# Kernel optimization log

Hardware: AMD Instinct MI355X
Metric: run time of the kernel (lower is better)

Reference implementation:

```python
import jax, jax.numpy as jnp
import numpy as np

N_EMBD = 1024
N_HEAD = 64

def setup_inputs() -> dict:
    key = jax.random.key(0)
    ks = jax.random.split(key, 7)
    B, T = 4, 4096
    x = jax.random.normal(ks[0], (B, T, N_EMBD), dtype=jnp.float32)
    # causal mask: True above the diagonal (masked positions)
    mask = jnp.triu(jnp.ones((T, T), dtype=bool), k=1)
    s = 1.0 / np.sqrt(N_EMBD)
    Wq = jax.random.normal(ks[1], (N_EMBD, N_HEAD), dtype=jnp.float32) * s
    bq = jnp.zeros((N_HEAD,), dtype=jnp.float32)
    Wk = jax.random.normal(ks[2], (N_EMBD, N_HEAD), dtype=jnp.float32) * s
    bk = jnp.zeros((N_HEAD,), dtype=jnp.float32)
    Wv = jax.random.normal(ks[3], (N_EMBD, N_HEAD), dtype=jnp.float32) * s
    bv = jnp.zeros((N_HEAD,), dtype=jnp.float32)
    return {"x": x, "mask": mask, "Wq": Wq, "bq": bq, "Wk": Wk, "bk": bk, "Wv": Wv, "bv": bv}

def reference(x, mask, Wq, bq, Wk, bk, Wv, bv):
    # x: [B,T,C], mask: [T,T] bool (True = masked)
    q = x @ Wq + bq            # [B,T,H]
    k = x @ Wk + bk            # [B,T,H]
    v = x @ Wv + bv            # [B,T,H]
    scale = 1.0 / jnp.sqrt(jnp.asarray(q.shape[-1], dtype=q.dtype))
    att = jnp.einsum('bth,bsh->bts', q, k) * scale   # [B,T,T]
    att = jnp.where(mask[None, :, :], -jnp.inf, att)
    att = jax.nn.softmax(att, axis=-1)
    # dropout omitted (eval mode / deterministic reference)
    return jnp.einsum('bts,bsh->bth', att, v)        # [B,T,H]
```

## Files before the change

### kernel.cpp

```cpp
#include <hip/hip_runtime.h>
#include <hip/hip_bf16.h>

#define BB 4
#define TT 4096
#define CC 1024
#define HH 64

#define QSCALE 0.18033688011112042f
#define FIXMAX2 23.083120654223414f

typedef __attribute__((ext_vector_type(8))) short short8;
typedef __attribute__((ext_vector_type(8))) ushort ushortx8;
typedef __attribute__((ext_vector_type(4))) float floatx4;

__device__ __forceinline__ ushort f2bf(float f) {
    union { float f; unsigned u; } a; a.f = f;
    const unsigned u = a.u;
    return (ushort)((u + 0x7fffu + ((u >> 16) & 1u)) >> 16);
}
__device__ __forceinline__ float bf2f(ushort h) {
    union { unsigned u; float f; } a; a.u = ((unsigned)h) << 16; return a.f;
}
__device__ __forceinline__ void load_lds16(const ushort* g, ushort* l) {
    __builtin_amdgcn_global_load_lds(
        (const __attribute__((address_space(1))) unsigned int*)g,
        (__attribute__((address_space(3))) unsigned int*)l, 16, 0, 0);
}

__global__ __launch_bounds__(256)
void wtrans_kernel(const float* __restrict__ Wq, const float* __restrict__ Wk,
                   const float* __restrict__ Wv, ushort* __restrict__ wT)
{
    __shared__ ushort tile[64 * 72];
    const int tid = threadIdx.x;
    const int mat = blockIdx.x >> 4, kt = blockIdx.x & 15;
    const float* W = (mat == 0) ? Wq : (mat == 1) ? Wk : Wv;
    #pragma unroll
    for (int it = 0; it < 16; ++it) {
        const int idx = it * 256 + tid;
        const int r = idx >> 6, c = idx & 63;
        tile[c * 72 + r] = f2bf(W[(size_t)(kt * 64 + r) * 64 + c]);
    }
    __syncthreads();
    #pragma unroll
    for (int it = 0; it < 16; ++it) {
        const int idx = it * 256 + tid;
        const int n = idx >> 6, kk = idx & 63;
        wT[((size_t)mat * 64 + n) * 1024 + kt * 64 + kk] = tile[n * 72 + kk];
    }
}

__global__ __launch_bounds__(256)
void qkv_mfma_kernel(const float* __restrict__ x, const ushort* __restrict__ wT,
                     const float* __restrict__ bq, const float* __restrict__ bk,
                     const float* __restrict__ bv,
                     ushort* __restrict__ q, ushort* __restrict__ k,
                     ushort* __restrict__ vT)
{
    __shared__ ushort xs [2][32 * 72];
    __shared__ ushort ws_[2][192 * 64];

    const int tid = threadIdx.x, w = tid >> 6, lane = tid & 63;
    const int m = lane & 15, quad = lane >> 4;
    const int row0 = blockIdx.x * 32;

    floatx4 acc[2][3];
    #pragma unroll
    for (int mi = 0; mi < 2; ++mi)
        #pragma unroll
        for (int j = 0; j < 3; ++j) acc[mi][j] = (floatx4){0.f, 0.f, 0.f, 0.f};

    const int lrow = lane >> 3;
    const int lg   = (lane & 7) ^ lrow;
    const ushort* gw = wT + (size_t)(w * 48 + lrow) * 1024 + lg * 8;

    const int xr = tid >> 3, xseg = tid & 7;
    const float* gx = x + (size_t)(row0 + xr) * CC + xseg * 8;

    int bslot[3][2];
    #pragma unroll
    for (int j = 0; j < 3; ++j)
        #pragma unroll
        for (int ks_ = 0; ks_ < 2; ++ks_)
            bslot[j][ks_] = ((w * 48 + j * 16 + m) * 8 +
                             ((ks_ * 4 + quad) ^ (m & 7))) * 8;

    {
        const float4 xa = *(const float4*)(gx);
        const float4 xb = *(const float4*)(gx + 4);
        #pragma unroll
        for (int j = 0; j < 6; ++j)
            load_lds16(gw + (size_t)j * 8192, &ws_[0][w * 3072 + j * 512]);
        ushortx8 p;
        p[0] = f2bf(xa.x); p[1] = f2bf(xa.y); p[2] = f2bf(xa.z); p[3] = f2bf(xa.w);
        p[4] = f2bf(xb.x); p[5] = f2bf(xb.y); p[6] = f2bf(xb.z); p[7] = f2bf(xb.w);
        *(ushortx8*)(&xs[0][xr * 72 + xseg * 8]) = p;
    }
    __syncthreads();

    for (int kc = 0; kc < 16; ++kc) {
        const int cur = kc & 1;
        float4 na, nb;
        if (kc < 15) {
            const int k0n = (kc + 1) * 64;
            na = *(const float4*)(gx + k0n);
            nb = *(const float4*)(gx + k0n + 4);
            #pragma unroll
            for (int j = 0; j < 6; ++j)
                load_lds16(gw + (size_t)j * 8192 + k0n, &ws_[cur ^ 1][w * 3072 + j * 512]);
        }
        const ushort* xb_ = xs[cur];
        const ushort* wb_ = ws_[cur];
        short8 bfr[3][2];
        #pragma unroll
        for (int j = 0; j < 3; ++j)
            #pragma unroll
            for (int ks_ = 0; ks_ < 2; ++ks_)
                bfr[j][ks_] = *(const short8*)(wb_ + bslot[j][ks_]);
        #pragma unroll
        for (int mi = 0; mi < 2; ++mi) {
            const short8 a0 = *(const short8*)(xb_ + (mi * 16 + m) * 72 + quad * 8);
            const short8 a1 = *(const short8*)(xb_ + (mi * 16 + m) * 72 + 32 + quad * 8);
            #pragma unroll
            for (int j = 0; j < 3; ++j) {
                acc[mi][j] = __builtin_amdgcn_mfma_f32_16x16x32_bf16(a0, bfr[j][0], acc[mi][j], 0, 0, 0);
                acc[mi][j] = __builtin_amdgcn_mfma_f32_16x16x32_bf16(a1, bfr[j][1], acc[mi][j], 0, 0, 0);
            }
        }
        if (kc < 15) {
            ushortx8 p;
            p[0] = f2bf(na.x); p[1] = f2bf(na.y); p[2] = f2bf(na.z); p[3] = f2bf(na.w);
            p[4] = f2bf(nb.x); p[5] = f2bf(nb.y); p[6] = f2bf(nb.z); p[7] = f2bf(nb.w);
            *(ushortx8*)(&xs[cur ^ 1][xr * 72 + xseg * 8]) = p;
        }
        __syncthreads();
    }

    const int b_ = row0 >> 12, tb = row0 & (TT - 1);
    #pragma unroll
    for (int j = 0; j < 3; ++j) {
        const int nt = w * 3 + j;
        const int mat = nt >> 2;
        const int c = (nt & 3) * 16 + m;
        const float bias = (mat == 0) ? bq[c] : (mat == 1) ? bk[c] : bv[c];
        #pragma unroll
        for (int mi = 0; mi < 2; ++mi) {
            const int gr0 = row0 + mi * 16 + quad * 4;
            if (mat == 0) {
                #pragma unroll
                for (int r = 0; r < 4; ++r)
                    q[(size_t)(gr0 + r) * HH + c] = f2bf((acc[mi][j][r] + bias) * QSCALE);
            } else if (mat == 1) {
                #pragma unroll
                for (int r = 0; r < 4; ++r)
                    k[(size_t)(gr0 + r) * HH + c] = f2bf(acc[mi][j][r] + bias);
            } else {
                ushort4 pv;
                pv.x = f2bf(acc[mi][j][0] + bias); pv.y = f2bf(acc[mi][j][1] + bias);
                pv.z = f2bf(acc[mi][j][2] + bias); pv.w = f2bf(acc[mi][j][3] + bias);
                const int t0 = tb + mi * 16 + quad * 4;
                *(ushort4*)(vT + ((size_t)b_ * HH + c) * TT + t0) = pv;
            }
        }
    }
}

__global__ __launch_bounds__(256)
void attn_mfma_kernel(const ushort* __restrict__ q, const ushort* __restrict__ k,
                      const ushort* __restrict__ vT,
                      float* __restrict__ partL, ushort* __restrict__ partO)
{
    __shared__ ushort ks[64 * 72];
    __shared__ ushort vs[64 * 72];
    __shared__ ushort ps[4][16 * 72];

    const int tid = threadIdx.x, w = tid >> 6, lane = tid & 63;
    const int m = lane & 15, quad = lane >> 4;
    const int pid = blockIdx.x;
    const int job = pid >> 3, split = pid & 7;
    const int b = job >> 6, tile = job & 63;
    const int i0 = tile * 64;
    const int nch = tile + 1;
    const int lo = (nch * split) >> 3, hi = (nch * (split + 1)) >> 3;

    const size_t qrow = ((size_t)b * TT + i0 + w * 16 + m) * HH;
    const uint4 aq0u = *(const uint4*)(q + qrow + quad * 8);
    const uint4 aq1u = *(const uint4*)(q + qrow + 32 + quad * 8);
    const short8 aq0 = *(const short8*)&aq0u;
    const short8 aq1 = *(const short8*)&aq1u;

    float lrow[4] = {0.f, 0.f, 0.f, 0.f};
    floatx4 oacc[4];
    #pragma unroll
    for (int nt = 0; nt < 4; ++nt) oacc[nt] = (floatx4){0.f, 0.f, 0.f, 0.f};

    const int iq0 = i0 + w * 16;
    for (int ch = lo; ch < hi; ++ch) {
        const int s0 = ch * 64;
        __syncthreads();
        const size_t kb = ((size_t)b * TT + s0) * HH;
        #pragma unroll
        for (int it = 0; it < 2; ++it) {
            const int t2 = it * 256 + tid;
            const int r = t2 >> 3, seg = t2 & 7;
            *(uint4*)(ks + r * 72 + seg * 8) = *(const uint4*)(k + kb + (size_t)r * HH + seg * 8);
            *(uint4*)(vs + r * 72 + seg * 8) = *(const uint4*)(vT + ((size_t)b * HH + r) * TT + s0 + seg * 8);
        }
        __syncthreads();

        floatx4 sc[4];
        #pragma unroll
        for (int nt = 0; nt < 4; ++nt) {
            const short8 b0 = *(const short8*)(ks + (nt * 16 + m) * 72 + quad * 8);
            const short8 b1 = *(const short8*)(ks + (nt * 16 + m) * 72 + 32 + quad * 8);
            floatx4 s_ = (floatx4){0.f, 0.f, 0.f, 0.f};
            s_ = __builtin_amdgcn_mfma_f32_16x16x32_bf16(aq0, b0, s_, 0, 0, 0);
            s_ = __builtin_amdgcn_mfma_f32_16x16x32_bf16(aq1, b1, s_, 0, 0, 0);
            sc[nt] = s_;
        }

        const bool need_mask = (s0 + 63 > iq0);
        #pragma unroll
        for (int r = 0; r < 4; ++r) {
            float t0 = sc[0][r] - FIXMAX2;
            float t1 = sc[1][r] - FIXMAX2;
            float t2 = sc[2][r] - FIXMAX2;
            float t3 = sc[3][r] - FIXMAX2;
            if (need_mask) {
                const int dlim = iq0 + quad * 4 + r - s0 - m;
                if (0  > dlim) t0 = -1e30f;
                if (16 > dlim) t1 = -1e30f;
                if (32 > dlim) t2 = -1e30f;
                if (48 > dlim) t3 = -1e30f;
            }
            const float p0 = __builtin_amdgcn_exp2f(t0);
            const float p1 = __builtin_amdgcn_exp2f(t1);
            const float p2 = __builtin_amdgcn_exp2f(t2);
            const float p3 = __builtin_amdgcn_exp2f(t3);
            lrow[r] += (p0 + p1) + (p2 + p3);
            ushort* pr = ps[w] + (quad * 4 + r) * 72;
            pr[m]      = f2bf(p0);
            pr[16 + m] = f2bf(p1);
            pr[32 + m] = f2bf(p2);
            pr[48 + m] = f2bf(p3);
        }

        #pragma unroll
        for (int ks_ = 0; ks_ < 2; ++ks_) {
            const short8 ap = *(const short8*)(ps[w] + m * 72 + ks_ * 32 + quad * 8);
            #pragma unroll
            for (int nt = 0; nt < 4; ++nt) {
                const short8 bv_ = *(const short8*)(vs + (nt * 16 + m) * 72 + ks_ * 32 + quad * 8);
                oacc[nt] = __builtin_amdgcn_mfma_f32_16x16x32_bf16(ap, bv_, oacc[nt], 0, 0, 0);
            }
        }
    }

    #pragma unroll
    for (int r = 0; r < 4; ++r) {
        float s = lrow[r];
        s += __shfl_xor(s, 1); s += __shfl_xor(s, 2);
        s += __shfl_xor(s, 4); s += __shfl_xor(s, 8);
        lrow[r] = s;
    }
    if (m == 0) {
        #pragma unroll
        for (int r = 0; r < 4; ++r)
            partL[(size_t)pid * 64 + w * 16 + quad * 4 + r] = lrow[r];
    }
    ushort* po = partO + ((size_t)pid * 64 + w * 16) * 64;
    #pragma unroll
    for (int r = 0; r < 4; ++r) {
        const int row = quad * 4 + r;
        #pragma unroll
        for (int nt = 0; nt < 4; ++nt)
            po[row * 64 + nt * 16 + m] = f2bf(oacc[nt][r]);
    }
}

__global__ __launch_bounds__(256)
void attn_combine_kernel(const float* __restrict__ partL,
                         const ushort* __restrict__ partO, float* __restrict__ out)
{
    const int job = blockIdx.x;
    const int tid = threadIdx.x;
    const int row = tid >> 2, dq = tid & 3;

    float L = 0.f;
    #pragma unroll
    for (int s = 0; s < 8; ++s) L += partL[(size_t)(job * 8 + s) * 64 + row];
    const float inv = 1.f / L;

    float o[16];
    #pragma unroll
    for (int i = 0; i < 16; ++i) o[i] = 0.f;
    #pragma unroll
    for (int s = 0; s < 8; ++s) {
        const ushort* po = partO + (((size_t)(job * 8 + s) * 64 + row) * 64 + dq * 16);
        #pragma unroll
        for (int i2 = 0; i2 < 2; ++i2) {
            const ushort4 pa = *(const ushort4*)(po + i2 * 8);
            const ushort4 pb = *(const ushort4*)(po + i2 * 8 + 4);
            o[i2*8+0] += bf2f(pa.x); o[i2*8+1] += bf2f(pa.y);
            o[i2*8+2] += bf2f(pa.z); o[i2*8+3] += bf2f(pa.w);
            o[i2*8+4] += bf2f(pb.x); o[i2*8+5] += bf2f(pb.y);
            o[i2*8+6] += bf2f(pb.z); o[i2*8+7] += bf2f(pb.w);
        }
    }
    float4* dst = (float4*)(out + ((size_t)job * 64 + row) * 64 + dq * 16);
    #pragma unroll
    for (int i = 0; i < 4; ++i) {
        float4 v; v.x = o[i*4]*inv; v.y = o[i*4+1]*inv; v.z = o[i*4+2]*inv; v.w = o[i*4+3]*inv;
        dst[i] = v;
    }
}

extern "C" void kernel_launch(void* const* d_in, const int* in_sizes, int n_in,
                              void* d_out, int out_size, void* d_ws, size_t ws_size,
                              hipStream_t stream) {
    (void)in_sizes; (void)n_in; (void)out_size; (void)ws_size;
    const float* x  = (const float*)d_in[0];
    const float* Wq = (const float*)d_in[2];
    const float* bq = (const float*)d_in[3];
    const float* Wk = (const float*)d_in[4];
    const float* bk = (const float*)d_in[5];
    const float* Wv = (const float*)d_in[6];
    const float* bv = (const float*)d_in[7];
    float* out = (float*)d_out;

    char* ws = (char*)d_ws;
    ushort* wT    = (ushort*)ws;
    ushort* qb    = (ushort*)(ws + 393216);
    ushort* kb    = qb + (size_t)BB * TT * HH;
    ushort* vTb   = kb + (size_t)BB * TT * HH;
    float*  partL = (float*) (ws + 6684672);
    ushort* partO = (ushort*)(ws + 7208960);

    wtrans_kernel   <<<48, 256, 0, stream>>>(Wq, Wk, Wv, wT);
    qkv_mfma_kernel <<<(BB * TT) / 32, 256, 0, stream>>>(x, wT, bq, bk, bv, qb, kb, vTb);
    attn_mfma_kernel<<<BB * 64 * 8, 256, 0, stream>>>(qb, kb, vTb, partL, partO);
    attn_combine_kernel<<<BB * 64, 256, 0, stream>>>(partL, partO, out);
}
```

Before: 200.3 us.

## Pre-swizzle weights into MFMA fragment order and load B fragments directly to registers

The weight transpose kernel now writes bf16 weights already arranged in per-lane MFMA B-fragment order. The QKV projection kernel reads these fragments straight from global memory into registers, double-buffered across k-chunks, instead of staging them through LDS with global_load_lds and swizzled reads. This removes the LDS traffic and LDS footprint for weights but adds register pressure and relies on L2 hits for the weight reads repeated by every block. The transpose kernel does uncoalesced strided reads, but it is small.

```diff
diff --git a/kernel.cpp b/kernel.cpp
--- a/kernel.cpp
+++ b/kernel.cpp
@@ -21,44 +21,41 @@
 __device__ __forceinline__ float bf2f(ushort h) {
     union { unsigned u; float f; } a; a.u = ((unsigned)h) << 16; return a.f;
 }
-__device__ __forceinline__ void load_lds16(const ushort* g, ushort* l) {
-    __builtin_amdgcn_global_load_lds(
-        (const __attribute__((address_space(1))) unsigned int*)g,
-        (__attribute__((address_space(3))) unsigned int*)l, 16, 0, 0);
-}
 
 __global__ __launch_bounds__(256)
 void wtrans_kernel(const float* __restrict__ Wq, const float* __restrict__ Wk,
-                   const float* __restrict__ Wv, ushort* __restrict__ wT)
+                   const float* __restrict__ Wv, ushort* __restrict__ wTf)
 {
-    __shared__ ushort tile[64 * 72];
     const int tid = threadIdx.x;
-    const int mat = blockIdx.x >> 4, kt = blockIdx.x & 15;
-    const float* W = (mat == 0) ? Wq : (mat == 1) ? Wk : Wv;
-    #pragma unroll
-    for (int it = 0; it < 16; ++it) {
-        const int idx = it * 256 + tid;
-        const int r = idx >> 6, c = idx & 63;
-        tile[c * 72 + r] = f2bf(W[(size_t)(kt * 64 + r) * 64 + c]);
-    }
-    __syncthreads();
-    #pragma unroll
-    for (int it = 0; it < 16; ++it) {
-        const int idx = it * 256 + tid;
-        const int n = idx >> 6, kk = idx & 63;
-        wT[((size_t)mat * 64 + n) * 1024 + kt * 64 + kk] = tile[n * 72 + kk];
+    const int kc = blockIdx.x;
+    #pragma unroll
+    for (int it = 0; it < 6; ++it) {
+        const int s = it * 256 + tid;
+        const int lane = s & 63;
+        const int t = s >> 6;
+        const int j = t % 3;
+        const int qv = t / 3;
+        const int wv = qv & 3, ks = qv >> 2;
+        const int r = wv * 48 + j * 16 + (lane & 15);
+        const int mat = r >> 6, n = r & 63;
+        const int k0 = kc * 64 + ks * 32 + (lane >> 4) * 8;
+        const float* W = (mat == 0) ? Wq : (mat == 1) ? Wk : Wv;
+        ushortx8 o;
+        #pragma unroll
+        for (int e = 0; e < 8; ++e)
+            o[e] = f2bf(W[(size_t)(k0 + e) * 64 + n]);
+        *(ushortx8*)(wTf + ((size_t)(kc * 24 + t) * 64 + lane) * 8) = o;
     }
 }
 
 __global__ __launch_bounds__(256)
-void qkv_mfma_kernel(const float* __restrict__ x, const ushort* __restrict__ wT,
+void qkv_mfma_kernel(const float* __restrict__ x, const ushort* __restrict__ wTf,
                      const float* __restrict__ bq, const float* __restrict__ bk,
                      const float* __restrict__ bv,
                      ushort* __restrict__ q, ushort* __restrict__ k,
                      ushort* __restrict__ vT)
 {
-    __shared__ ushort xs [2][32 * 72];
-    __shared__ ushort ws_[2][192 * 64];
+    __shared__ ushort xs[2][32 * 72];
 
     const int tid = threadIdx.x, w = tid >> 6, lane = tid & 63;
     const int m = lane & 15, quad = lane >> 4;
@@ -70,27 +67,21 @@
         #pragma unroll
         for (int j = 0; j < 3; ++j) acc[mi][j] = (floatx4){0.f, 0.f, 0.f, 0.f};
 
-    const int lrow = lane >> 3;
-    const int lg   = (lane & 7) ^ lrow;
-    const ushort* gw = wT + (size_t)(w * 48 + lrow) * 1024 + lg * 8;
+    const ushort* gb = wTf + (size_t)w * 1536 + lane * 8;
 
     const int xr = tid >> 3, xseg = tid & 7;
     const float* gx = x + (size_t)(row0 + xr) * CC + xseg * 8;
 
-    int bslot[3][2];
+    short8 bcur[3][2], bnxt[3][2];
+
     #pragma unroll
     for (int j = 0; j < 3; ++j)
         #pragma unroll
         for (int ks_ = 0; ks_ < 2; ++ks_)
-            bslot[j][ks_] = ((w * 48 + j * 16 + m) * 8 +
-                             ((ks_ * 4 + quad) ^ (m & 7))) * 8;
-
+            bcur[j][ks_] = *(const short8*)(gb + ks_ * 6144 + j * 512);
     {
         const float4 xa = *(const float4*)(gx);
         const float4 xb = *(const float4*)(gx + 4);
-        #pragma unroll
-        for (int j = 0; j < 6; ++j)
-            load_lds16(gw + (size_t)j * 8192, &ws_[0][w * 3072 + j * 512]);
         ushortx8 p;
         p[0] = f2bf(xa.x); p[1] = f2bf(xa.y); p[2] = f2bf(xa.z); p[3] = f2bf(xa.w);
         p[4] = f2bf(xb.x); p[5] = f2bf(xb.y); p[6] = f2bf(xb.z); p[7] = f2bf(xb.w);
@@ -105,26 +96,22 @@
             const int k0n = (kc + 1) * 64;
             na = *(const float4*)(gx + k0n);
             nb = *(const float4*)(gx + k0n + 4);
+            const ushort* gn = gb + (size_t)(kc + 1) * 12288;
             #pragma unroll
-            for (int j = 0; j < 6; ++j)
-                load_lds16(gw + (size_t)j * 8192 + k0n, &ws_[cur ^ 1][w * 3072 + j * 512]);
+            for (int j = 0; j < 3; ++j)
+                #pragma unroll
+                for (int ks_ = 0; ks_ < 2; ++ks_)
+                    bnxt[j][ks_] = *(const short8*)(gn + ks_ * 6144 + j * 512);
         }
         const ushort* xb_ = xs[cur];
-        const ushort* wb_ = ws_[cur];
-        short8 bfr[3][2];
-        #pragma unroll
-        for (int j = 0; j < 3; ++j)
-            #pragma unroll
-            for (int ks_ = 0; ks_ < 2; ++ks_)
-                bfr[j][ks_] = *(const short8*)(wb_ + bslot[j][ks_]);
         #pragma unroll
         for (int mi = 0; mi < 2; ++mi) {
             const short8 a0 = *(const short8*)(xb_ + (mi * 16 + m) * 72 + quad * 8);
             const short8 a1 = *(const short8*)(xb_ + (mi * 16 + m) * 72 + 32 + quad * 8);
             #pragma unroll
             for (int j = 0; j < 3; ++j) {
-                acc[mi][j] = __builtin_amdgcn_mfma_f32_16x16x32_bf16(a0, bfr[j][0], acc[mi][j], 0, 0, 0);
-                acc[mi][j] = __builtin_amdgcn_mfma_f32_16x16x32_bf16(a1, bfr[j][1], acc[mi][j], 0, 0, 0);
+                acc[mi][j] = __builtin_amdgcn_mfma_f32_16x16x32_bf16(a0, bcur[j][0], acc[mi][j], 0, 0, 0);
+                acc[mi][j] = __builtin_amdgcn_mfma_f32_16x16x32_bf16(a1, bcur[j][1], acc[mi][j], 0, 0, 0);
             }
         }
         if (kc < 15) {
@@ -132,6 +119,11 @@
             p[0] = f2bf(na.x); p[1] = f2bf(na.y); p[2] = f2bf(na.z); p[3] = f2bf(na.w);
             p[4] = f2bf(nb.x); p[5] = f2bf(nb.y); p[6] = f2bf(nb.z); p[7] = f2bf(nb.w);
             *(ushortx8*)(&xs[cur ^ 1][xr * 72 + xseg * 8]) = p;
+            #pragma unroll
+            for (int j = 0; j < 3; ++j) {
+                bcur[j][0] = bnxt[j][0];
+                bcur[j][1] = bnxt[j][1];
+            }
         }
         __syncthreads();
     }
@@ -329,15 +321,15 @@
     float* out = (float*)d_out;
 
     char* ws = (char*)d_ws;
-    ushort* wT    = (ushort*)ws;
+    ushort* wTf   = (ushort*)ws;
     ushort* qb    = (ushort*)(ws + 393216);
     ushort* kb    = qb + (size_t)BB * TT * HH;
     ushort* vTb   = kb + (size_t)BB * TT * HH;
     float*  partL = (float*) (ws + 6684672);
     ushort* partO = (ushort*)(ws + 7208960);
 
-    wtrans_kernel   <<<48, 256, 0, stream>>>(Wq, Wk, Wv, wT);
-    qkv_mfma_kernel <<<(BB * TT) / 32, 256, 0, stream>>>(x, wT, bq, bk, bv, qb, kb, vTb);
+    wtrans_kernel   <<<16, 256, 0, stream>>>(Wq, Wk, Wv, wTf);
+    qkv_mfma_kernel <<<(BB * TT) / 32, 256, 0, stream>>>(x, wTf, bq, bk, bv, qb, kb, vTb);
     attn_mfma_kernel<<<BB * 64 * 8, 256, 0, stream>>>(qb, kb, vTb, partL, partO);
     attn_combine_kernel<<<BB * 64, 256, 0, stream>>>(partL, partO, out);
 }
```

New measurement: 196.4 us. Within noise of the previous version (-1.9%).
